# Kernel tuning notes

Hardware: AMD Instinct MI355X
Metric: run time of the kernel (lower is better)

The kernel has to match this reference:

```python
import jax, jax.numpy as jnp
import numpy as np
from jax import lax

B, T, N, NIN, NOUT = 16, 32, 512, 32, 16
STEEP_GJ, STEEP_FIRE, STEEP_IN = 10.0, 10.0, 5.0
INPUT_THRESH, LEAKY_SLOPE = 0.01, 0.01
EDGE_P = 0.05


def setup_inputs() -> dict:
    key = jax.random.key(0)
    ks = jax.random.split(key, 7)
    obs_sequence = jax.random.normal(ks[0], (B, T, NIN), dtype=jnp.float32)
    weights = jax.random.uniform(ks[1], (N, N), dtype=jnp.float32) * 5.0
    thresholds = jax.random.uniform(ks[2], (N,), dtype=jnp.float32) * 5.0
    decay = jax.random.uniform(ks[3], (N,), dtype=jnp.float32) * 0.5
    mask_ex = jax.random.bernoulli(ks[4], EDGE_P, (N, N)).astype(jnp.float32)
    mask_in = jax.random.bernoulli(ks[5], EDGE_P, (N, N)).astype(jnp.float32)
    mask_gj = jax.random.bernoulli(ks[6], EDGE_P, (N, N)).astype(jnp.float32)
    input_indices = jnp.arange(NIN, dtype=jnp.int32)
    output_indices = NIN + jnp.arange(NOUT, dtype=jnp.int32)
    return {"obs_sequence": obs_sequence, "weights": weights, "thresholds": thresholds,
            "decay": decay, "mask_ex": mask_ex, "mask_in": mask_in, "mask_gj": mask_gj,
            "input_indices": input_indices, "output_indices": output_indices}


def reference(obs_sequence, weights, thresholds, decay, mask_ex, mask_in, mask_gj,
              input_indices, output_indices):
    # obs_encoder and action_decoder are identity: obs values drive input neurons,
    # action = E-state of output neurons.
    W_pos = jax.nn.softplus(weights)            # [N,N] (dst, src)
    W_chem = W_pos * (mask_ex - mask_in)        # excitatory minus inhibitory
    W_gj = W_pos * mask_gj                      # gap junctions

    def step(carry, obs_t):
        E, O = carry                            # [B,N] each
        O_h = O.at[:, input_indices].set(obs_t)
        E_h = E.at[:, input_indices].set(obs_t)
        # chemical synapse current: [B,N] @ [N,N]^T
        I_chem = O_h @ W_chem.T
        # gap junction current via O(B,N,N) broadcast, as in original
        diff = O_h[:, None, :] - E_h[:, :, None]          # [B, dst, src]
        direction = jnp.tanh(STEEP_GJ * diff)
        I_gj = jnp.einsum('ds,bs,bds->bd', W_gj, O_h, direction)
        curr = jnp.clip(E_h + I_chem + I_gj, -10.0, 10.0)
        z = curr - thresholds
        O_new = jnp.where(z >= 0, z, LEAKY_SLOPE * z)      # leaky_relu
        firing_gate = jax.nn.sigmoid(STEEP_FIRE * z)
        decay_gate = jax.nn.sigmoid(STEEP_IN * (jnp.abs(E_h - curr) - INPUT_THRESH))
        E_nonfired = decay_gate * curr + (1.0 - decay_gate) * (E_h - decay)
        E_new = firing_gate * O_new + (1.0 - firing_gate) * E_nonfired
        O_new = O_new.at[:, input_indices].set(obs_t)
        E_new = E_new.at[:, input_indices].set(obs_t)
        action = E_new[:, output_indices]
        return (E_new, O_new), action

    b, n = obs_sequence.shape[0], weights.shape[0]
    E0 = jnp.zeros((b, n), dtype=obs_sequence.dtype)
    O0 = jnp.zeros((b, n), dtype=obs_sequence.dtype)
    (_, _), actions = lax.scan(step, (E0, O0), jnp.swapaxes(obs_sequence, 0, 1))
    return jnp.swapaxes(actions, 0, 1)                    # [B,T,NOUT]
```

## Files before the change

### kernel.cpp

```cpp
#include <hip/hip_runtime.h>

#define N_NEUR 512
#define B_SZ   16
#define T_STEPS 32
#define NIN    32
#define NOUT   16
#define CAPC   84
#define CAPG   52
#define MC     42
#define MG     26
#define MCP    21
#define MGP    13
#define LOG2E  1.4426950408889634f

__device__ __forceinline__ float rcp_fast(float x) {
#if __has_builtin(__builtin_amdgcn_rcpf)
    return __builtin_amdgcn_rcpf(x);
#else
    return 1.0f / x;
#endif
}
__device__ __forceinline__ float exp2_fast(float x) {
#if __has_builtin(__builtin_amdgcn_exp2f)
    return __builtin_amdgcn_exp2f(x);
#else
    return exp2f(x);
#endif
}

__global__ __launch_bounds__(64) void prep1_kernel(
    const float* __restrict__ W,
    const float* __restrict__ mex,
    const float* __restrict__ min_,
    const float* __restrict__ mgj,
    int* __restrict__ key_arr, int* __restrict__ ccA, int* __restrict__ cgA,
    int2* __restrict__ tmpC, int2* __restrict__ tmpG)
{
    const int row  = blockIdx.x;
    const int lane = threadIdx.x;
    const unsigned long long below = (1ull << lane) - 1ull;
    int bc = 0, bg = 0;
    for (int c0 = 0; c0 < N_NEUR; c0 += 64) {
        const int col = c0 + lane;
        const int off = row * N_NEUR + col;
        const float w  = W[off];
        const float sp = fmaxf(w, 0.0f) + log1pf(__expf(-fabsf(w)));
        const float dm = mex[off] - min_[off];
        bool a = (dm != 0.0f);
        unsigned long long m = __ballot(a);
        int idx = bc + __popcll(m & below);
        if (a && idx < CAPC)
            tmpC[row * CAPC + idx] = make_int2(col, __float_as_int(sp * dm));
        bc += __popcll(m);

        const float g = mgj[off];
        bool ag = (g != 0.0f);
        m = __ballot(ag);
        idx = bg + __popcll(m & below);
        if (ag && idx < CAPG)
            tmpG[row * CAPG + idx] = make_int2(col, __float_as_int(sp * g));
        bg += __popcll(m);
    }
    if (lane == 0) {
        int cc = min(bc, CAPC), cg = min(bg, CAPG);
        ccA[row] = cc; cgA[row] = cg; key_arr[row] = cc + cg;
    }
}

__global__ __launch_bounds__(64) void prep2_kernel(
    const int* __restrict__ key_arr, const int* __restrict__ ccA, const int* __restrict__ cgA,
    const int2* __restrict__ tmpC, const int2* __restrict__ tmpG,
    int* __restrict__ order,
    float* __restrict__ wCt, unsigned* __restrict__ cpCt,
    float* __restrict__ wGt, unsigned* __restrict__ cpGt)
{
    __shared__ int   cS[CAPC];  __shared__ float wS[CAPC];
    __shared__ int   cSg[CAPG]; __shared__ float wSg[CAPG];
    __shared__ int   keyS[MC];
    __shared__ int   scol[MC];  __shared__ float sw[MC];
    const int d    = blockIdx.x;
    const int lane = threadIdx.x;
    const int kd   = key_arr[d];
    int r = 0;
    for (int j = lane; j < N_NEUR; j += 64) {
        int kj = key_arr[j];
        r += (kj < kd) || (kj == kd && j < d);
    }
    #pragma unroll
    for (int i = 1; i < 64; i <<= 1) r += __shfl_xor(r, i);
    if (lane == 0) order[r] = d;

    const int wv = r >> 5;
    const int Lb = 2 * (r & 31);
    const int cc = ccA[d], cg = cgA[d];

    for (int k = lane; k < CAPC; k += 64) {
        int2 e = (k < cc) ? tmpC[d * CAPC + k] : make_int2(0, 0);
        cS[k] = e.x; wS[k] = __int_as_float(e.y);
    }
    for (int k = lane; k < CAPG; k += 64) {
        int2 e = (k < cg) ? tmpG[d * CAPG + k] : make_int2(0, 0);
        cSg[k] = e.x; wSg[k] = __int_as_float(e.y);
    }
    __syncthreads();

    #pragma unroll
    for (int task = 0; task < 4; ++task) {
        const int isG = task >> 1, h = task & 1;
        const int cnt = isG ? cg : cc;
        const int m   = (cnt + 1 - h) >> 1;
        const int M   = isG ? MG : MC;
        const int MP  = isG ? MGP : MCP;
        const int myL = Lb + h;

        int col = 0; float w = 0.0f; int key = 0;
        if (lane < m) {
            col = isG ? cSg[2 * lane + h] : cS[2 * lane + h];
            w   = isG ? wSg[2 * lane + h] : wS[2 * lane + h];
            key = ((col & 31) - myL) & 31;
            keyS[lane] = key;
        }
        __syncthreads();
        if (lane < m) {
            int rk = 0;
            for (int j = 0; j < m; ++j) {
                int kj = keyS[j];
                rk += (kj < key) || (kj == key && j < lane);
            }
            scol[rk] = col; sw[rk] = w;
        }
        __syncthreads();
        float*    wT = isG ? wGt  : wCt;
        unsigned* cT = isG ? cpGt : cpCt;
        if (lane < M)
            wT[(wv * M + lane) * 64 + myL] = (lane < m) ? sw[lane] : 0.0f;
        if (lane < MP) {
            unsigned c0 = (2 * lane     < m) ? ((unsigned)scol[2 * lane]     << 2) : 0u;
            unsigned c1 = (2 * lane + 1 < m) ? ((unsigned)scol[2 * lane + 1] << 2) : 0u;
            cT[(wv * MP + lane) * 64 + myL] = c0 | (c1 << 16);
        }
        __syncthreads();
    }
}

#define CHEM_K(k, A) {                                                      \
    unsigned pk = cpC[(k) >> 1];                                            \
    unsigned off = ((k) & 1) ? (pk >> 16) : (pk & 0xffffu);                 \
    A = fmaf(wC[k], *(const float*)((const char*)ObP + off), A); }

#define CHEM_C4(a) { CHEM_K(a, accA) CHEM_K((a)+1, accB) CHEM_K((a)+2, accA) CHEM_K((a)+3, accB) }

#define GJ_K(k, A) {                                                        \
    unsigned pk = cpG[(k) >> 1];                                            \
    unsigned off = ((k) & 1) ? (pk >> 16) : (pk & 0xffffu);                 \
    float Os = *(const float*)((const char*)ObP + off);                     \
    float f = fmaf(20.0f * LOG2E, Os, cE);                                  \
    float tnh = 1.0f - 2.0f * rcp_fast(1.0f + exp2_fast(f));                \
    A = fmaf(wG[k] * Os, tnh, A); }

#define GJ_C4(a) { GJ_K(a, accA) GJ_K((a)+1, accB) GJ_K((a)+2, accA) GJ_K((a)+3, accB) }

__global__ __launch_bounds__(1024, 1) void recur_kernel(
    const float* __restrict__ obs,
    const float* __restrict__ thr,
    const float* __restrict__ dec,
    const int* __restrict__ order, const int* __restrict__ ccA, const int* __restrict__ cgA,
    const float* __restrict__ wCt, const unsigned* __restrict__ cpCt,
    const float* __restrict__ wGt, const unsigned* __restrict__ cpGt,
    float* __restrict__ out)
{
    __shared__ float Ob[2][N_NEUR];
    __shared__ float Eb[2][N_NEUR];

    const int b    = blockIdx.x;
    const int tid  = threadIdx.x;
    const int h    = tid & 1;
    const int r    = tid >> 1;
    const int wv   = tid >> 6;
    const int lane = tid & 63;

    const int d = order[r];
    const int cc = ccA[d];
    const int cg = cgA[d];
    const float thr_d = thr[d];
    const float dec_d = dec[d];

    int ccw = cc, cgw = cg;
    #pragma unroll
    for (int i = 1; i < 64; i <<= 1) {
        ccw = max(ccw, __shfl_xor(ccw, i));
        cgw = max(cgw, __shfl_xor(cgw, i));
    }
    const int mCw = __builtin_amdgcn_readfirstlane((ccw + 1) >> 1);
    const int mGw = __builtin_amdgcn_readfirstlane((cgw + 1) >> 1);

    float wC[MC]; unsigned cpC[MCP];
    float wG[MG]; unsigned cpG[MGP];
    #pragma unroll
    for (int k = 0; k < MC; ++k)  wC[k]  = wCt[(wv * MC + k) * 64 + lane];
    #pragma unroll
    for (int k = 0; k < MCP; ++k) cpC[k] = cpCt[(wv * MCP + k) * 64 + lane];
    #pragma unroll
    for (int k = 0; k < MG; ++k)  wG[k]  = wGt[(wv * MG + k) * 64 + lane];
    #pragma unroll
    for (int k = 0; k < MGP; ++k) cpG[k] = cpGt[(wv * MGP + k) * 64 + lane];

    const bool inj = (h == 0) && (d < NIN);
    const bool wr  = (h == 0) && (d >= NIN) && (d < NIN + NOUT);
    float* outp = out + (size_t)b * T_STEPS * NOUT + (d - NIN);
    const float* obs_b = obs + b * (T_STEPS * NIN);

    if (h == 0) {
        float v = (d < NIN) ? obs_b[d] : 0.0f;
        Ob[0][d] = v;
        Eb[0][d] = v;
    }
    int p = 0;
    __syncthreads();

    for (int t = 0; t < T_STEPS; ++t) {
        float ob_next = (inj && (t + 1 < T_STEPS)) ? obs_b[(t + 1) * NIN + d] : 0.0f;

        const float* ObP = Ob[p];
        const float E_d = Eb[p][d];
        float accA = 0.0f, accB = 0.0f;
        CHEM_C4(0)
        if ( 4 < mCw) CHEM_C4(4)
        if ( 8 < mCw) CHEM_C4(8)
        if (12 < mCw) CHEM_C4(12)
        if (16 < mCw) CHEM_C4(16)
        if (20 < mCw) CHEM_C4(20)
        if (24 < mCw) CHEM_C4(24)
        if (28 < mCw) CHEM_C4(28)
        if (32 < mCw) CHEM_C4(32)
        if (36 < mCw) CHEM_C4(36)
        if (40 < mCw) { CHEM_K(40, accA) CHEM_K(41, accB) }
        const float cE = -20.0f * LOG2E * E_d;
        GJ_C4(0)
        if ( 4 < mGw) GJ_C4(4)
        if ( 8 < mGw) GJ_C4(8)
        if (12 < mGw) GJ_C4(12)
        if (16 < mGw) GJ_C4(16)
        if (20 < mGw) GJ_C4(20)
        if (24 < mGw) { GJ_K(24, accA) GJ_K(25, accB) }

        float acc = accA + accB;
        acc += __shfl_xor(acc, 1);

        float curr = fminf(fmaxf(E_d + acc, -10.0f), 10.0f);
        float z = curr - thr_d;
        float O_new = (z >= 0.0f) ? z : 0.01f * z;
        float fg = rcp_fast(1.0f + exp2_fast(-10.0f * LOG2E * z));
        float dg = rcp_fast(1.0f + exp2_fast(-5.0f * LOG2E * (fabsf(E_d - curr) - 0.01f)));
        float E_nf  = dg * curr + (1.0f - dg) * (E_d - dec_d);
        float E_new = fg * O_new + (1.0f - fg) * E_nf;

        const int q = p ^ 1;
        if (h == 0) {
            Eb[q][d] = inj ? ob_next : E_new;
            Ob[q][d] = inj ? ob_next : O_new;
            if (wr) outp[t * NOUT] = E_new;
        }
        __syncthreads();
        p = q;
    }
}

extern "C" void kernel_launch(void* const* d_in, const int* in_sizes, int n_in,
                              void* d_out, int out_size, void* d_ws, size_t ws_size,
                              hipStream_t stream)
{
    const float* obs  = (const float*)d_in[0];
    const float* W    = (const float*)d_in[1];
    const float* thr  = (const float*)d_in[2];
    const float* dec  = (const float*)d_in[3];
    const float* mex  = (const float*)d_in[4];
    const float* min_ = (const float*)d_in[5];
    const float* mgj  = (const float*)d_in[6];
    float* out = (float*)d_out;

    char* ws = (char*)d_ws;
    int*   key_arr = (int*)(ws);
    int*   ccA     = (int*)(ws + 2048);
    int*   cgA     = (int*)(ws + 4096);
    int*   order   = (int*)(ws + 6144);
    int2*  tmpC    = (int2*)(ws + 8192);
    int2*  tmpG    = (int2*)(ws + 8192 + 344064);
    float* wCt     = (float*)(ws + 565248);
    unsigned* cpCt = (unsigned*)(ws + 737280);
    float* wGt     = (float*)(ws + 823296);
    unsigned* cpGt = (unsigned*)(ws + 929792);

    prep1_kernel<<<N_NEUR, 64, 0, stream>>>(W, mex, min_, mgj,
                                            key_arr, ccA, cgA, tmpC, tmpG);
    prep2_kernel<<<N_NEUR, 64, 0, stream>>>(key_arr, ccA, cgA, tmpC, tmpG,
                                            order, wCt, cpCt, wGt, cpGt);
    recur_kernel<<<B_SZ, 1024, 0, stream>>>(obs, thr, dec,
                                            order, ccA, cgA,
                                            wCt, cpCt, wGt, cpGt, out);
}
```

Measured before the change: 186.4 us.

## Precompute ranks in separate kernel, spread edge slots to reduce LDS bank conflicts

Result: slower. 255.8 us (+37.2%).

```diff
diff --git a/kernel.cpp b/kernel.cpp
--- a/kernel.cpp
+++ b/kernel.cpp
@@ -25,6 +25,13 @@
     return __builtin_amdgcn_exp2f(x);
 #else
     return exp2f(x);
+#endif
+}
+__device__ __forceinline__ float pair_swap(float x) {
+#if __has_builtin(__builtin_amdgcn_mov_dpp)
+    return __int_as_float(__builtin_amdgcn_mov_dpp(__float_as_int(x), 0xB1, 0xF, 0xF, true));
+#else
+    return __shfl_xor(x, 1);
 #endif
 }
 
@@ -67,10 +74,39 @@
     }
 }
 
+__global__ __launch_bounds__(512) void rank_kernel(
+    int* __restrict__ key_then_rank,
+    const int* __restrict__ ccA, const int* __restrict__ cgA,
+    int* __restrict__ order, int* __restrict__ mCwA, int* __restrict__ mGwA)
+{
+    __shared__ int keyS[N_NEUR];
+    __shared__ int mxc[16], mxg[16];
+    const int d = threadIdx.x;
+    keyS[d] = key_then_rank[d];
+    if (d < 16) { mxc[d] = 0; mxg[d] = 0; }
+    __syncthreads();
+    const int kd = keyS[d];
+    int r = 0;
+    #pragma unroll 8
+    for (int j = 0; j < N_NEUR; ++j) {
+        int kj = keyS[j];
+        r += (kj < kd) || (kj == kd && j < d);
+    }
+    order[r] = d;
+    key_then_rank[d] = r;
+    atomicMax(&mxc[r >> 5], ccA[d]);
+    atomicMax(&mxg[r >> 5], cgA[d]);
+    __syncthreads();
+    if (d < 16) {
+        mCwA[d] = (mxc[d] + 1) >> 1;
+        mGwA[d] = (mxg[d] + 1) >> 1;
+    }
+}
+
 __global__ __launch_bounds__(64) void prep2_kernel(
-    const int* __restrict__ key_arr, const int* __restrict__ ccA, const int* __restrict__ cgA,
+    const int* __restrict__ rankA, const int* __restrict__ ccA, const int* __restrict__ cgA,
+    const int* __restrict__ mCwA, const int* __restrict__ mGwA,
     const int2* __restrict__ tmpC, const int2* __restrict__ tmpG,
-    int* __restrict__ order,
     float* __restrict__ wCt, unsigned* __restrict__ cpCt,
     float* __restrict__ wGt, unsigned* __restrict__ cpGt)
 {
@@ -78,21 +114,14 @@
     __shared__ int   cSg[CAPG]; __shared__ float wSg[CAPG];
     __shared__ int   keyS[MC];
     __shared__ int   scol[MC];  __shared__ float sw[MC];
+    __shared__ float wOut[MC];  __shared__ int   oOut[MC];
     const int d    = blockIdx.x;
     const int lane = threadIdx.x;
-    const int kd   = key_arr[d];
-    int r = 0;
-    for (int j = lane; j < N_NEUR; j += 64) {
-        int kj = key_arr[j];
-        r += (kj < kd) || (kj == kd && j < d);
-    }
-    #pragma unroll
-    for (int i = 1; i < 64; i <<= 1) r += __shfl_xor(r, i);
-    if (lane == 0) order[r] = d;
-
-    const int wv = r >> 5;
-    const int Lb = 2 * (r & 31);
+    const int r    = rankA[d];
+    const int wv   = r >> 5;
+    const int Lb   = 2 * (r & 31);
     const int cc = ccA[d], cg = cgA[d];
+    const int Mc = mCwA[wv], Mg = mGwA[wv];
 
     for (int k = lane; k < CAPC; k += 64) {
         int2 e = (k < cc) ? tmpC[d * CAPC + k] : make_int2(0, 0);
@@ -106,12 +135,13 @@
 
     #pragma unroll
     for (int task = 0; task < 4; ++task) {
-        const int isG = task >> 1, h = task & 1;
-        const int cnt = isG ? cg : cc;
-        const int m   = (cnt + 1 - h) >> 1;
-        const int M   = isG ? MG : MC;
-        const int MP  = isG ? MGP : MCP;
-        const int myL = Lb + h;
+        const int isG  = task >> 1, h = task & 1;
+        const int cnt  = isG ? cg : cc;
+        const int m    = (cnt + 1 - h) >> 1;
+        const int M    = isG ? Mg : Mc;
+        const int Mcap = isG ? MG : MC;
+        const int MPc  = isG ? MGP : MCP;
+        const int myL  = Lb + h;
 
         int col = 0; float w = 0.0f; int key = 0;
         if (lane < m) {
@@ -129,15 +159,36 @@
             }
             scol[rk] = col; sw[rk] = w;
         }
+        if (lane < Mcap) { wOut[lane] = 0.0f; oOut[lane] = 0; }
         __syncthreads();
+
+        int a = -(1 << 28);
+        int colj = 0; float wj = 0.0f;
+        if (lane < m) {
+            colj = scol[lane]; wj = sw[lane];
+            int kj = ((colj & 31) - myL) & 31;
+            a = ((kj * M) >> 5) - lane;
+        }
+        #pragma unroll
+        for (int o = 1; o < 64; o <<= 1) {
+            int t2 = __shfl_up(a, o);
+            if (lane >= o) a = max(a, t2);
+        }
+        if (lane < m) {
+            int slot = min(lane + a, M - m + lane);
+            wOut[slot] = wj;
+            oOut[slot] = colj << 2;
+        }
+        __syncthreads();
+
         float*    wT = isG ? wGt  : wCt;
         unsigned* cT = isG ? cpGt : cpCt;
-        if (lane < M)
-            wT[(wv * M + lane) * 64 + myL] = (lane < m) ? sw[lane] : 0.0f;
-        if (lane < MP) {
-            unsigned c0 = (2 * lane     < m) ? ((unsigned)scol[2 * lane]     << 2) : 0u;
-            unsigned c1 = (2 * lane + 1 < m) ? ((unsigned)scol[2 * lane + 1] << 2) : 0u;
-            cT[(wv * MP + lane) * 64 + myL] = c0 | (c1 << 16);
+        if (lane < Mcap)
+            wT[(wv * Mcap + lane) * 64 + myL] = wOut[lane];
+        if (lane < MPc) {
+            unsigned c0 = (unsigned)oOut[2 * lane];
+            unsigned c1 = (unsigned)oOut[2 * lane + 1];
+            cT[(wv * MPc + lane) * 64 + myL] = c0 | (c1 << 16);
         }
         __syncthreads();
     }
@@ -160,11 +211,53 @@
 
 #define GJ_C4(a) { GJ_K(a, accA) GJ_K((a)+1, accB) GJ_K((a)+2, accA) GJ_K((a)+3, accB) }
 
+#define STEP(t, P, Q) {                                                       \
+    float ob_next = (inj && ((t) + 1 < T_STEPS)) ? obs_b[((t) + 1) * NIN + d] : 0.0f; \
+    const float* ObP = Ob[P];                                                 \
+    const float E_d = Eb[P][d];                                               \
+    float accA = 0.0f, accB = 0.0f;                                           \
+    CHEM_C4(0)                                                                \
+    if ( 4 < mCw) CHEM_C4(4)                                                  \
+    if ( 8 < mCw) CHEM_C4(8)                                                  \
+    if (12 < mCw) CHEM_C4(12)                                                 \
+    if (16 < mCw) CHEM_C4(16)                                                 \
+    if (20 < mCw) CHEM_C4(20)                                                 \
+    if (24 < mCw) CHEM_C4(24)                                                 \
+    if (28 < mCw) CHEM_C4(28)                                                 \
+    if (32 < mCw) CHEM_C4(32)                                                 \
+    if (36 < mCw) CHEM_C4(36)                                                 \
+    if (40 < mCw) { CHEM_K(40, accA) CHEM_K(41, accB) }                       \
+    const float cE = -20.0f * LOG2E * E_d;                                    \
+    GJ_C4(0)                                                                  \
+    if ( 4 < mGw) GJ_C4(4)                                                    \
+    if ( 8 < mGw) GJ_C4(8)                                                    \
+    if (12 < mGw) GJ_C4(12)                                                   \
+    if (16 < mGw) GJ_C4(16)                                                   \
+    if (20 < mGw) GJ_C4(20)                                                   \
+    if (24 < mGw) { GJ_K(24, accA) GJ_K(25, accB) }                           \
+    float acc = accA + accB;                                                  \
+    acc += pair_swap(acc);                                                    \
+    float curr = fminf(fmaxf(E_d + acc, -10.0f), 10.0f);                      \
+    float z = curr - thr_d;                                                   \
+    float O_new = (z >= 0.0f) ? z : 0.01f * z;                                \
+    float fg = rcp_fast(1.0f + exp2_fast(-10.0f * LOG2E * z));                \
+    float dg = rcp_fast(1.0f + exp2_fast(-5.0f * LOG2E * (fabsf(E_d - curr) - 0.01f))); \
+    float E_nf  = dg * curr + (1.0f - dg) * (E_d - dec_d);                    \
+    float E_new = fg * O_new + (1.0f - fg) * E_nf;                            \
+    if (h == 0) {                                                             \
+        Eb[Q][d] = inj ? ob_next : E_new;                                     \
+        Ob[Q][d] = inj ? ob_next : O_new;                                     \
+        if (wr) outp[(t) * NOUT] = E_new;                                     \
+    }                                                                         \
+    __syncthreads();                                                          \
+}
+
 __global__ __launch_bounds__(1024, 1) void recur_kernel(
     const float* __restrict__ obs,
     const float* __restrict__ thr,
     const float* __restrict__ dec,
-    const int* __restrict__ order, const int* __restrict__ ccA, const int* __restrict__ cgA,
+    const int* __restrict__ order,
+    const int* __restrict__ mCwA, const int* __restrict__ mGwA,
     const float* __restrict__ wCt, const unsigned* __restrict__ cpCt,
     const float* __restrict__ wGt, const unsigned* __restrict__ cpGt,
     float* __restrict__ out)
@@ -180,19 +273,11 @@
     const int lane = tid & 63;
 
     const int d = order[r];
-    const int cc = ccA[d];
-    const int cg = cgA[d];
     const float thr_d = thr[d];
     const float dec_d = dec[d];
 
-    int ccw = cc, cgw = cg;
-    #pragma unroll
-    for (int i = 1; i < 64; i <<= 1) {
-        ccw = max(ccw, __shfl_xor(ccw, i));
-        cgw = max(cgw, __shfl_xor(cgw, i));
-    }
-    const int mCw = __builtin_amdgcn_readfirstlane((ccw + 1) >> 1);
-    const int mGw = __builtin_amdgcn_readfirstlane((cgw + 1) >> 1);
+    const int mCw = __builtin_amdgcn_readfirstlane(mCwA[wv]);
+    const int mGw = __builtin_amdgcn_readfirstlane(mGwA[wv]);
 
     float wC[MC]; unsigned cpC[MCP];
     float wG[MG]; unsigned cpG[MGP];
@@ -215,54 +300,11 @@
         Ob[0][d] = v;
         Eb[0][d] = v;
     }
-    int p = 0;
     __syncthreads();
 
-    for (int t = 0; t < T_STEPS; ++t) {
-        float ob_next = (inj && (t + 1 < T_STEPS)) ? obs_b[(t + 1) * NIN + d] : 0.0f;
-
-        const float* ObP = Ob[p];
-        const float E_d = Eb[p][d];
-        float accA = 0.0f, accB = 0.0f;
-        CHEM_C4(0)
-        if ( 4 < mCw) CHEM_C4(4)
-        if ( 8 < mCw) CHEM_C4(8)
-        if (12 < mCw) CHEM_C4(12)
-        if (16 < mCw) CHEM_C4(16)
-        if (20 < mCw) CHEM_C4(20)
-        if (24 < mCw) CHEM_C4(24)
-        if (28 < mCw) CHEM_C4(28)
-        if (32 < mCw) CHEM_C4(32)
-        if (36 < mCw) CHEM_C4(36)
-        if (40 < mCw) { CHEM_K(40, accA) CHEM_K(41, accB) }
-        const float cE = -20.0f * LOG2E * E_d;
-        GJ_C4(0)
-        if ( 4 < mGw) GJ_C4(4)
-        if ( 8 < mGw) GJ_C4(8)
-        if (12 < mGw) GJ_C4(12)
-        if (16 < mGw) GJ_C4(16)
-        if (20 < mGw) GJ_C4(20)
-        if (24 < mGw) { GJ_K(24, accA) GJ_K(25, accB) }
-
-        float acc = accA + accB;
-        acc += __shfl_xor(acc, 1);
-
-        float curr = fminf(fmaxf(E_d + acc, -10.0f), 10.0f);
-        float z = curr - thr_d;
-        float O_new = (z >= 0.0f) ? z : 0.01f * z;
-        float fg = rcp_fast(1.0f + exp2_fast(-10.0f * LOG2E * z));
-        float dg = rcp_fast(1.0f + exp2_fast(-5.0f * LOG2E * (fabsf(E_d - curr) - 0.01f)));
-        float E_nf  = dg * curr + (1.0f - dg) * (E_d - dec_d);
-        float E_new = fg * O_new + (1.0f - fg) * E_nf;
-
-        const int q = p ^ 1;
-        if (h == 0) {
-            Eb[q][d] = inj ? ob_next : E_new;
-            Ob[q][d] = inj ? ob_next : O_new;
-            if (wr) outp[t * NOUT] = E_new;
-        }
-        __syncthreads();
-        p = q;
+    for (int t = 0; t < T_STEPS; t += 2) {
+        STEP(t,     0, 1)
+        STEP(t + 1, 1, 0)
     }
 }
 
@@ -290,12 +332,15 @@
     unsigned* cpCt = (unsigned*)(ws + 737280);
     float* wGt     = (float*)(ws + 823296);
     unsigned* cpGt = (unsigned*)(ws + 929792);
+    int*   mCwA    = (int*)(ws + 983040);
+    int*   mGwA    = (int*)(ws + 983104);
 
     prep1_kernel<<<N_NEUR, 64, 0, stream>>>(W, mex, min_, mgj,
                                             key_arr, ccA, cgA, tmpC, tmpG);
-    prep2_kernel<<<N_NEUR, 64, 0, stream>>>(key_arr, ccA, cgA, tmpC, tmpG,
-                                            order, wCt, cpCt, wGt, cpGt);
+    rank_kernel<<<1, 512, 0, stream>>>(key_arr, ccA, cgA, order, mCwA, mGwA);
+    prep2_kernel<<<N_NEUR, 64, 0, stream>>>(key_arr, ccA, cgA, mCwA, mGwA,
+                                            tmpC, tmpG, wCt, cpCt, wGt, cpGt);
     recur_kernel<<<B_SZ, 1024, 0, stream>>>(obs, thr, dec,
-                                            order, ccA, cgA,
+                                            order, mCwA, mGwA,
                                             wCt, cpCt, wGt, cpGt, out);
 }
```

## Fuse prep and recurrence kernels into one cooperative kernel with grid syncs

Applied to the files above, without the earlier changes.

Result: slower. 254.9 us (+36.8%).

```diff
diff --git a/kernel.cpp b/kernel.cpp
--- a/kernel.cpp
+++ b/kernel.cpp
@@ -1,4 +1,6 @@
 #include <hip/hip_runtime.h>
+#include <hip/hip_cooperative_groups.h>
+namespace cg = cooperative_groups;
 
 #define N_NEUR 512
 #define B_SZ   16
@@ -11,6 +13,7 @@
 #define MG     26
 #define MCP    21
 #define MGP    13
+#define NWAVE  16
 #define LOG2E  1.4426950408889634f
 
 __device__ __forceinline__ float rcp_fast(float x) {
@@ -27,120 +30,12 @@
     return exp2f(x);
 #endif
 }
-
-__global__ __launch_bounds__(64) void prep1_kernel(
-    const float* __restrict__ W,
-    const float* __restrict__ mex,
-    const float* __restrict__ min_,
-    const float* __restrict__ mgj,
-    int* __restrict__ key_arr, int* __restrict__ ccA, int* __restrict__ cgA,
-    int2* __restrict__ tmpC, int2* __restrict__ tmpG)
-{
-    const int row  = blockIdx.x;
-    const int lane = threadIdx.x;
-    const unsigned long long below = (1ull << lane) - 1ull;
-    int bc = 0, bg = 0;
-    for (int c0 = 0; c0 < N_NEUR; c0 += 64) {
-        const int col = c0 + lane;
-        const int off = row * N_NEUR + col;
-        const float w  = W[off];
-        const float sp = fmaxf(w, 0.0f) + log1pf(__expf(-fabsf(w)));
-        const float dm = mex[off] - min_[off];
-        bool a = (dm != 0.0f);
-        unsigned long long m = __ballot(a);
-        int idx = bc + __popcll(m & below);
-        if (a && idx < CAPC)
-            tmpC[row * CAPC + idx] = make_int2(col, __float_as_int(sp * dm));
-        bc += __popcll(m);
-
-        const float g = mgj[off];
-        bool ag = (g != 0.0f);
-        m = __ballot(ag);
-        idx = bg + __popcll(m & below);
-        if (ag && idx < CAPG)
-            tmpG[row * CAPG + idx] = make_int2(col, __float_as_int(sp * g));
-        bg += __popcll(m);
-    }
-    if (lane == 0) {
-        int cc = min(bc, CAPC), cg = min(bg, CAPG);
-        ccA[row] = cc; cgA[row] = cg; key_arr[row] = cc + cg;
-    }
-}
-
-__global__ __launch_bounds__(64) void prep2_kernel(
-    const int* __restrict__ key_arr, const int* __restrict__ ccA, const int* __restrict__ cgA,
-    const int2* __restrict__ tmpC, const int2* __restrict__ tmpG,
-    int* __restrict__ order,
-    float* __restrict__ wCt, unsigned* __restrict__ cpCt,
-    float* __restrict__ wGt, unsigned* __restrict__ cpGt)
-{
-    __shared__ int   cS[CAPC];  __shared__ float wS[CAPC];
-    __shared__ int   cSg[CAPG]; __shared__ float wSg[CAPG];
-    __shared__ int   keyS[MC];
-    __shared__ int   scol[MC];  __shared__ float sw[MC];
-    const int d    = blockIdx.x;
-    const int lane = threadIdx.x;
-    const int kd   = key_arr[d];
-    int r = 0;
-    for (int j = lane; j < N_NEUR; j += 64) {
-        int kj = key_arr[j];
-        r += (kj < kd) || (kj == kd && j < d);
-    }
-    #pragma unroll
-    for (int i = 1; i < 64; i <<= 1) r += __shfl_xor(r, i);
-    if (lane == 0) order[r] = d;
-
-    const int wv = r >> 5;
-    const int Lb = 2 * (r & 31);
-    const int cc = ccA[d], cg = cgA[d];
-
-    for (int k = lane; k < CAPC; k += 64) {
-        int2 e = (k < cc) ? tmpC[d * CAPC + k] : make_int2(0, 0);
-        cS[k] = e.x; wS[k] = __int_as_float(e.y);
-    }
-    for (int k = lane; k < CAPG; k += 64) {
-        int2 e = (k < cg) ? tmpG[d * CAPG + k] : make_int2(0, 0);
-        cSg[k] = e.x; wSg[k] = __int_as_float(e.y);
-    }
-    __syncthreads();
-
-    #pragma unroll
-    for (int task = 0; task < 4; ++task) {
-        const int isG = task >> 1, h = task & 1;
-        const int cnt = isG ? cg : cc;
-        const int m   = (cnt + 1 - h) >> 1;
-        const int M   = isG ? MG : MC;
-        const int MP  = isG ? MGP : MCP;
-        const int myL = Lb + h;
-
-        int col = 0; float w = 0.0f; int key = 0;
-        if (lane < m) {
-            col = isG ? cSg[2 * lane + h] : cS[2 * lane + h];
-            w   = isG ? wSg[2 * lane + h] : wS[2 * lane + h];
-            key = ((col & 31) - myL) & 31;
-            keyS[lane] = key;
-        }
-        __syncthreads();
-        if (lane < m) {
-            int rk = 0;
-            for (int j = 0; j < m; ++j) {
-                int kj = keyS[j];
-                rk += (kj < key) || (kj == key && j < lane);
-            }
-            scol[rk] = col; sw[rk] = w;
-        }
-        __syncthreads();
-        float*    wT = isG ? wGt  : wCt;
-        unsigned* cT = isG ? cpGt : cpCt;
-        if (lane < M)
-            wT[(wv * M + lane) * 64 + myL] = (lane < m) ? sw[lane] : 0.0f;
-        if (lane < MP) {
-            unsigned c0 = (2 * lane     < m) ? ((unsigned)scol[2 * lane]     << 2) : 0u;
-            unsigned c1 = (2 * lane + 1 < m) ? ((unsigned)scol[2 * lane + 1] << 2) : 0u;
-            cT[(wv * MP + lane) * 64 + myL] = c0 | (c1 << 16);
-        }
-        __syncthreads();
-    }
+__device__ __forceinline__ float pair_swap(float x) {
+#if __has_builtin(__builtin_amdgcn_mov_dpp)
+    return __int_as_float(__builtin_amdgcn_mov_dpp(__float_as_int(x), 0xB1, 0xF, 0xF, true));
+#else
+    return __shfl_xor(x, 1);
+#endif
 }
 
 #define CHEM_K(k, A) {                                                      \
@@ -160,32 +55,166 @@
 
 #define GJ_C4(a) { GJ_K(a, accA) GJ_K((a)+1, accB) GJ_K((a)+2, accA) GJ_K((a)+3, accB) }
 
-__global__ __launch_bounds__(1024, 1) void recur_kernel(
+__global__ __launch_bounds__(1024, 1) void fused_kernel(
     const float* __restrict__ obs,
+    const float* __restrict__ W,
     const float* __restrict__ thr,
     const float* __restrict__ dec,
-    const int* __restrict__ order, const int* __restrict__ ccA, const int* __restrict__ cgA,
-    const float* __restrict__ wCt, const unsigned* __restrict__ cpCt,
-    const float* __restrict__ wGt, const unsigned* __restrict__ cpGt,
-    float* __restrict__ out)
+    const float* __restrict__ mex,
+    const float* __restrict__ min_,
+    const float* __restrict__ mgj,
+    float* __restrict__ out,
+    char* __restrict__ ws)
 {
+    int*      key_arr = (int*)(ws);
+    int*      ccA     = (int*)(ws + 2048);
+    int*      cgA     = (int*)(ws + 4096);
+    int2*     tmpC    = (int2*)(ws + 8192);
+    int2*     tmpG    = (int2*)(ws + 8192 + 344064);
+    float*    wCt     = (float*)(ws + 565248);
+    unsigned* cpCt    = (unsigned*)(ws + 737280);
+    float*    wGt     = (float*)(ws + 823296);
+    unsigned* cpGt    = (unsigned*)(ws + 929792);
+
     __shared__ float Ob[2][N_NEUR];
     __shared__ float Eb[2][N_NEUR];
+    __shared__ int   keyS[N_NEUR];
+    __shared__ int   orderS[N_NEUR];
+    __shared__ int   rankS[N_NEUR];
+    __shared__ int   pcC[NWAVE][CAPC]; __shared__ float pwC[NWAVE][CAPC];
+    __shared__ int   pcG[NWAVE][CAPG]; __shared__ float pwG[NWAVE][CAPG];
+    __shared__ int   pkey[NWAVE][MC];
+    __shared__ int   pscol[NWAVE][MC]; __shared__ float psw[NWAVE][MC];
+
+    cg::grid_group grid = cg::this_grid();
 
     const int b    = blockIdx.x;
     const int tid  = threadIdx.x;
-    const int h    = tid & 1;
-    const int r    = tid >> 1;
     const int wv   = tid >> 6;
     const int lane = tid & 63;
 
-    const int d = order[r];
+    int ccR[2], cgR[2];
+    {
+        const unsigned long long below = (1ull << lane) - 1ull;
+        const int g = b * NWAVE + wv;
+        for (int rr = 0; rr < 2; ++rr) {
+            const int row = 2 * g + rr;
+            int bc = 0, bg = 0;
+            for (int c0 = 0; c0 < N_NEUR; c0 += 64) {
+                const int col = c0 + lane;
+                const int off = row * N_NEUR + col;
+                const float w  = W[off];
+                const float sp = fmaxf(w, 0.0f) + log1pf(__expf(-fabsf(w)));
+                const float dm = mex[off] - min_[off];
+                bool a = (dm != 0.0f);
+                unsigned long long m = __ballot(a);
+                int idx = bc + __popcll(m & below);
+                if (a && idx < CAPC)
+                    tmpC[row * CAPC + idx] = make_int2(col, __float_as_int(sp * dm));
+                bc += __popcll(m);
+
+                const float gj = mgj[off];
+                bool ag = (gj != 0.0f);
+                m = __ballot(ag);
+                idx = bg + __popcll(m & below);
+                if (ag && idx < CAPG)
+                    tmpG[row * CAPG + idx] = make_int2(col, __float_as_int(sp * gj));
+                bg += __popcll(m);
+            }
+            ccR[rr] = min(bc, CAPC); cgR[rr] = min(bg, CAPG);
+            if (lane == 0) {
+                ccA[row] = ccR[rr]; cgA[row] = cgR[rr];
+                key_arr[row] = ccR[rr] + cgR[rr];
+            }
+        }
+    }
+    grid.sync();
+
+    if (tid < N_NEUR) keyS[tid] = key_arr[tid];
+    __syncthreads();
+    if (tid < N_NEUR) {
+        const int kd = keyS[tid];
+        int r = 0;
+        #pragma unroll 8
+        for (int j = 0; j < N_NEUR; ++j) {
+            int kj = keyS[j];
+            r += (kj < kd) || (kj == kd && j < tid);
+        }
+        orderS[r] = tid;
+        rankS[tid] = r;
+    }
+    __syncthreads();
+
+    {
+        const int g = b * NWAVE + wv;
+        for (int rr = 0; rr < 2; ++rr) {
+            const int row = 2 * g + rr;
+            const int r   = rankS[row];
+            const int wvT = r >> 5;
+            const int Lb  = 2 * (r & 31);
+            const int cc  = ccR[rr], cgj = cgR[rr];
+
+            for (int k = lane; k < CAPC; k += 64) {
+                int2 e = (k < cc) ? tmpC[row * CAPC + k] : make_int2(0, 0);
+                pcC[wv][k] = e.x; pwC[wv][k] = __int_as_float(e.y);
+            }
+            for (int k = lane; k < CAPG; k += 64) {
+                int2 e = (k < cgj) ? tmpG[row * CAPG + k] : make_int2(0, 0);
+                pcG[wv][k] = e.x; pwG[wv][k] = __int_as_float(e.y);
+            }
+            __syncthreads();
+
+            #pragma unroll
+            for (int task = 0; task < 4; ++task) {
+                const int isG  = task >> 1, h = task & 1;
+                const int cnt  = isG ? cgj : cc;
+                const int m    = (cnt + 1 - h) >> 1;
+                const int Mcap = isG ? MG : MC;
+                const int MPc  = isG ? MGP : MCP;
+                const int myL  = Lb + h;
+
+                int col = 0; float wgt = 0.0f; int key = 0;
+                if (lane < m) {
+                    col = isG ? pcG[wv][2 * lane + h] : pcC[wv][2 * lane + h];
+                    wgt = isG ? pwG[wv][2 * lane + h] : pwC[wv][2 * lane + h];
+                    key = ((col & 31) - myL) & 31;
+                    pkey[wv][lane] = key;
+                }
+                __syncthreads();
+                if (lane < m) {
+                    int rk = 0;
+                    for (int j = 0; j < m; ++j) {
+                        int kj = pkey[wv][j];
+                        rk += (kj < key) || (kj == key && j < lane);
+                    }
+                    pscol[wv][rk] = col; psw[wv][rk] = wgt;
+                }
+                __syncthreads();
+                float*    wT = isG ? wGt  : wCt;
+                unsigned* cT = isG ? cpGt : cpCt;
+                if (lane < Mcap)
+                    wT[(wvT * Mcap + lane) * 64 + myL] = (lane < m) ? psw[wv][lane] : 0.0f;
+                if (lane < MPc) {
+                    unsigned c0 = (2 * lane     < m) ? ((unsigned)pscol[wv][2 * lane]     << 2) : 0u;
+                    unsigned c1 = (2 * lane + 1 < m) ? ((unsigned)pscol[wv][2 * lane + 1] << 2) : 0u;
+                    cT[(wvT * MPc + lane) * 64 + myL] = c0 | (c1 << 16);
+                }
+                __syncthreads();
+            }
+        }
+    }
+    grid.sync();
+
+    const int h = tid & 1;
+    const int r = tid >> 1;
+
+    const int d = orderS[r];
     const int cc = ccA[d];
-    const int cg = cgA[d];
+    const int cgj = cgA[d];
     const float thr_d = thr[d];
     const float dec_d = dec[d];
 
-    int ccw = cc, cgw = cg;
+    int ccw = cc, cgw = cgj;
     #pragma unroll
     for (int i = 1; i < 64; i <<= 1) {
         ccw = max(ccw, __shfl_xor(ccw, i));
@@ -245,7 +274,7 @@
         if (24 < mGw) { GJ_K(24, accA) GJ_K(25, accB) }
 
         float acc = accA + accB;
-        acc += __shfl_xor(acc, 1);
+        acc += pair_swap(acc);
 
         float curr = fminf(fmaxf(E_d + acc, -10.0f), 10.0f);
         float z = curr - thr_d;
@@ -278,24 +307,12 @@
     const float* min_ = (const float*)d_in[5];
     const float* mgj  = (const float*)d_in[6];
     float* out = (float*)d_out;
-
     char* ws = (char*)d_ws;
-    int*   key_arr = (int*)(ws);
-    int*   ccA     = (int*)(ws + 2048);
-    int*   cgA     = (int*)(ws + 4096);
-    int*   order   = (int*)(ws + 6144);
-    int2*  tmpC    = (int2*)(ws + 8192);
-    int2*  tmpG    = (int2*)(ws + 8192 + 344064);
-    float* wCt     = (float*)(ws + 565248);
-    unsigned* cpCt = (unsigned*)(ws + 737280);
-    float* wGt     = (float*)(ws + 823296);
-    unsigned* cpGt = (unsigned*)(ws + 929792);
-
-    prep1_kernel<<<N_NEUR, 64, 0, stream>>>(W, mex, min_, mgj,
-                                            key_arr, ccA, cgA, tmpC, tmpG);
-    prep2_kernel<<<N_NEUR, 64, 0, stream>>>(key_arr, ccA, cgA, tmpC, tmpG,
-                                            order, wCt, cpCt, wGt, cpGt);
-    recur_kernel<<<B_SZ, 1024, 0, stream>>>(obs, thr, dec,
-                                            order, ccA, cgA,
-                                            wCt, cpCt, wGt, cpGt, out);
-}
+
+    void* args[] = {
+        (void*)&obs, (void*)&W, (void*)&thr, (void*)&dec,
+        (void*)&mex, (void*)&min_, (void*)&mgj, (void*)&out, (void*)&ws
+    };
+    hipLaunchCooperativeKernel((const void*)fused_kernel,
+                               dim3(B_SZ), dim3(1024), args, 0, stream);
+}
```

## Stream synapse weights from global memory as float2 pairs instead of registers

Applied to the files above, without the earlier changes.

New measurement: 198.4 us. +6.5%, slower.

```diff
diff --git a/kernel.cpp b/kernel.cpp
--- a/kernel.cpp
+++ b/kernel.cpp
@@ -25,6 +25,13 @@
     return __builtin_amdgcn_exp2f(x);
 #else
     return exp2f(x);
+#endif
+}
+__device__ __forceinline__ float pair_swap(float x) {
+#if __has_builtin(__builtin_amdgcn_mov_dpp)
+    return __int_as_float(__builtin_amdgcn_mov_dpp(__float_as_int(x), 0xB1, 0xF, 0xF, true));
+#else
+    return __shfl_xor(x, 1);
 #endif
 }
 
@@ -71,8 +78,8 @@
     const int* __restrict__ key_arr, const int* __restrict__ ccA, const int* __restrict__ cgA,
     const int2* __restrict__ tmpC, const int2* __restrict__ tmpG,
     int* __restrict__ order,
-    float* __restrict__ wCt, unsigned* __restrict__ cpCt,
-    float* __restrict__ wGt, unsigned* __restrict__ cpGt)
+    float2* __restrict__ wCt, unsigned* __restrict__ cpCt,
+    float2* __restrict__ wGt, unsigned* __restrict__ cpGt)
 {
     __shared__ int   cS[CAPC];  __shared__ float wS[CAPC];
     __shared__ int   cSg[CAPG]; __shared__ float wSg[CAPG];
@@ -109,7 +116,6 @@
         const int isG = task >> 1, h = task & 1;
         const int cnt = isG ? cg : cc;
         const int m   = (cnt + 1 - h) >> 1;
-        const int M   = isG ? MG : MC;
         const int MP  = isG ? MGP : MCP;
         const int myL = Lb + h;
 
@@ -130,11 +136,13 @@
             scol[rk] = col; sw[rk] = w;
         }
         __syncthreads();
-        float*    wT = isG ? wGt  : wCt;
+        float2*   wT = isG ? wGt  : wCt;
         unsigned* cT = isG ? cpGt : cpCt;
-        if (lane < M)
-            wT[(wv * M + lane) * 64 + myL] = (lane < m) ? sw[lane] : 0.0f;
         if (lane < MP) {
+            float2 v;
+            v.x = (2 * lane     < m) ? sw[2 * lane]     : 0.0f;
+            v.y = (2 * lane + 1 < m) ? sw[2 * lane + 1] : 0.0f;
+            wT[(wv * MP + lane) * 64 + myL] = v;
             unsigned c0 = (2 * lane     < m) ? ((unsigned)scol[2 * lane]     << 2) : 0u;
             unsigned c1 = (2 * lane + 1 < m) ? ((unsigned)scol[2 * lane + 1] << 2) : 0u;
             cT[(wv * MP + lane) * 64 + myL] = c0 | (c1 << 16);
@@ -143,30 +151,31 @@
     }
 }
 
-#define CHEM_K(k, A) {                                                      \
-    unsigned pk = cpC[(k) >> 1];                                            \
-    unsigned off = ((k) & 1) ? (pk >> 16) : (pk & 0xffffu);                 \
-    A = fmaf(wC[k], *(const float*)((const char*)ObP + off), A); }
-
-#define CHEM_C4(a) { CHEM_K(a, accA) CHEM_K((a)+1, accB) CHEM_K((a)+2, accA) CHEM_K((a)+3, accB) }
-
-#define GJ_K(k, A) {                                                        \
-    unsigned pk = cpG[(k) >> 1];                                            \
-    unsigned off = ((k) & 1) ? (pk >> 16) : (pk & 0xffffu);                 \
-    float Os = *(const float*)((const char*)ObP + off);                     \
-    float f = fmaf(20.0f * LOG2E, Os, cE);                                  \
-    float tnh = 1.0f - 2.0f * rcp_fast(1.0f + exp2_fast(f));                \
-    A = fmaf(wG[k] * Os, tnh, A); }
-
-#define GJ_C4(a) { GJ_K(a, accA) GJ_K((a)+1, accB) GJ_K((a)+2, accA) GJ_K((a)+3, accB) }
+#define CHEM_P(kp) {                                                        \
+    unsigned pk = cpC[kp];                                                  \
+    float2 wp = wCb[(kp) * 64];                                             \
+    accA = fmaf(wp.x, *(const float*)((const char*)ObP + (pk & 0xffffu)), accA); \
+    accB = fmaf(wp.y, *(const float*)((const char*)ObP + (pk >> 16)), accB); }
+
+#define GJ_P(kp) {                                                         \
+    unsigned pk = cpG[kp];                                                 \
+    float2 wp = wGb[(kp) * 64];                                            \
+    {   float Os = *(const float*)((const char*)ObP + (pk & 0xffffu));     \
+        float f = fmaf(20.0f * LOG2E, Os, cE);                             \
+        float tnh = 1.0f - 2.0f * rcp_fast(1.0f + exp2_fast(f));           \
+        accA = fmaf(wp.x * Os, tnh, accA); }                               \
+    {   float Os = *(const float*)((const char*)ObP + (pk >> 16));         \
+        float f = fmaf(20.0f * LOG2E, Os, cE);                             \
+        float tnh = 1.0f - 2.0f * rcp_fast(1.0f + exp2_fast(f));           \
+        accB = fmaf(wp.y * Os, tnh, accB); } }
 
 __global__ __launch_bounds__(1024, 1) void recur_kernel(
     const float* __restrict__ obs,
     const float* __restrict__ thr,
     const float* __restrict__ dec,
     const int* __restrict__ order, const int* __restrict__ ccA, const int* __restrict__ cgA,
-    const float* __restrict__ wCt, const unsigned* __restrict__ cpCt,
-    const float* __restrict__ wGt, const unsigned* __restrict__ cpGt,
+    const float2* __restrict__ wCt, const unsigned* __restrict__ cpCt,
+    const float2* __restrict__ wGt, const unsigned* __restrict__ cpGt,
     float* __restrict__ out)
 {
     __shared__ float Ob[2][N_NEUR];
@@ -194,16 +203,14 @@
     const int mCw = __builtin_amdgcn_readfirstlane((ccw + 1) >> 1);
     const int mGw = __builtin_amdgcn_readfirstlane((cgw + 1) >> 1);
 
-    float wC[MC]; unsigned cpC[MCP];
-    float wG[MG]; unsigned cpG[MGP];
-    #pragma unroll
-    for (int k = 0; k < MC; ++k)  wC[k]  = wCt[(wv * MC + k) * 64 + lane];
+    unsigned cpC[MCP]; unsigned cpG[MGP];
     #pragma unroll
     for (int k = 0; k < MCP; ++k) cpC[k] = cpCt[(wv * MCP + k) * 64 + lane];
     #pragma unroll
-    for (int k = 0; k < MG; ++k)  wG[k]  = wGt[(wv * MG + k) * 64 + lane];
-    #pragma unroll
     for (int k = 0; k < MGP; ++k) cpG[k] = cpGt[(wv * MGP + k) * 64 + lane];
+
+    const float2* wCb = wCt + (wv * MCP) * 64 + lane;
+    const float2* wGb = wGt + (wv * MGP) * 64 + lane;
 
     const bool inj = (h == 0) && (d < NIN);
     const bool wr  = (h == 0) && (d >= NIN) && (d < NIN + NOUT);
@@ -224,28 +231,28 @@
         const float* ObP = Ob[p];
         const float E_d = Eb[p][d];
         float accA = 0.0f, accB = 0.0f;
-        CHEM_C4(0)
-        if ( 4 < mCw) CHEM_C4(4)
-        if ( 8 < mCw) CHEM_C4(8)
-        if (12 < mCw) CHEM_C4(12)
-        if (16 < mCw) CHEM_C4(16)
-        if (20 < mCw) CHEM_C4(20)
-        if (24 < mCw) CHEM_C4(24)
-        if (28 < mCw) CHEM_C4(28)
-        if (32 < mCw) CHEM_C4(32)
-        if (36 < mCw) CHEM_C4(36)
-        if (40 < mCw) { CHEM_K(40, accA) CHEM_K(41, accB) }
+        CHEM_P(0)  CHEM_P(1)
+        if ( 4 < mCw) { CHEM_P(2)  CHEM_P(3)  }
+        if ( 8 < mCw) { CHEM_P(4)  CHEM_P(5)  }
+        if (12 < mCw) { CHEM_P(6)  CHEM_P(7)  }
+        if (16 < mCw) { CHEM_P(8)  CHEM_P(9)  }
+        if (20 < mCw) { CHEM_P(10) CHEM_P(11) }
+        if (24 < mCw) { CHEM_P(12) CHEM_P(13) }
+        if (28 < mCw) { CHEM_P(14) CHEM_P(15) }
+        if (32 < mCw) { CHEM_P(16) CHEM_P(17) }
+        if (36 < mCw) { CHEM_P(18) CHEM_P(19) }
+        if (40 < mCw) { CHEM_P(20) }
         const float cE = -20.0f * LOG2E * E_d;
-        GJ_C4(0)
-        if ( 4 < mGw) GJ_C4(4)
-        if ( 8 < mGw) GJ_C4(8)
-        if (12 < mGw) GJ_C4(12)
-        if (16 < mGw) GJ_C4(16)
-        if (20 < mGw) GJ_C4(20)
-        if (24 < mGw) { GJ_K(24, accA) GJ_K(25, accB) }
+        GJ_P(0)  GJ_P(1)
+        if ( 4 < mGw) { GJ_P(2)  GJ_P(3)  }
+        if ( 8 < mGw) { GJ_P(4)  GJ_P(5)  }
+        if (12 < mGw) { GJ_P(6)  GJ_P(7)  }
+        if (16 < mGw) { GJ_P(8)  GJ_P(9)  }
+        if (20 < mGw) { GJ_P(10) GJ_P(11) }
+        if (24 < mGw) { GJ_P(12) }
 
         float acc = accA + accB;
-        acc += __shfl_xor(acc, 1);
+        acc += pair_swap(acc);
 
         float curr = fminf(fmaxf(E_d + acc, -10.0f), 10.0f);
         float z = curr - thr_d;
@@ -286,9 +293,9 @@
     int*   order   = (int*)(ws + 6144);
     int2*  tmpC    = (int2*)(ws + 8192);
     int2*  tmpG    = (int2*)(ws + 8192 + 344064);
-    float* wCt     = (float*)(ws + 565248);
+    float2* wCt    = (float2*)(ws + 565248);
     unsigned* cpCt = (unsigned*)(ws + 737280);
-    float* wGt     = (float*)(ws + 823296);
+    float2* wGt    = (float2*)(ws + 823296);
     unsigned* cpGt = (unsigned*)(ws + 929792);
 
     prep1_kernel<<<N_NEUR, 64, 0, stream>>>(W, mex, min_, mgj,
```
